# Kernel optimization log

Measured on AMD Instinct MI355X. Metric: run time of the kernel, lower is better.

Reference implementation:

```python
import jax, jax.numpy as jnp
import numpy as np

B, N, H = 1, 4096, 2048
NH, HD = 16, H // 16
WINDOW = 4096
EPS = 1e-6
THETA = 10000.0
NEG = -1e30


def rmsnorm(x, w):
    var = jnp.mean(jnp.square(x.astype(jnp.float32)), axis=-1, keepdims=True)
    return (x * jax.lax.rsqrt(var + EPS)).astype(w.dtype) * w


def rotate_half(x):
    x1, x2 = x[..., : x.shape[-1] // 2], x[..., x.shape[-1] // 2 :]
    return jnp.concatenate((-x2, x1), axis=-1)


def setup_inputs() -> dict:
    key = jax.random.key(0)
    k1, k2, k3 = jax.random.split(key, 3)
    x = jax.random.normal(k1, (B, N, H), dtype=jnp.float32)
    w_qkv = jax.random.normal(k2, (H, 3 * H), dtype=jnp.float32) * (1.0 / np.sqrt(H))
    w_out = jax.random.normal(k3, (H, H), dtype=jnp.float32) * (1.0 / np.sqrt(H))
    q_gamma = jnp.ones((HD,), dtype=jnp.float32)
    k_gamma = jnp.ones((HD,), dtype=jnp.float32)
    return {"x": x, "w_qkv": w_qkv, "w_out": w_out, "q_gamma": q_gamma, "k_gamma": k_gamma}


def reference(x, w_qkv, w_out, q_gamma, k_gamma):
    b, n, _ = x.shape
    qkv = jnp.einsum('bnh,hm->bnm', x, w_qkv)  # [b,n,3H]
    q, k, v = jnp.split(qkv, 3, axis=-1)
    # [b, nh, n, hd]
    q = q.reshape(b, n, NH, HD).transpose(0, 2, 1, 3)
    k = k.reshape(b, n, NH, HD).transpose(0, 2, 1, 3)
    v = v.reshape(b, n, NH, HD).transpose(0, 2, 1, 3)
    # qk RMSNorm over head_dim
    q = rmsnorm(q, q_gamma)
    k = rmsnorm(k, k_gamma)
    # RoPE
    inv_freq = 1.0 / (THETA ** (jnp.arange(0, HD, 2, dtype=jnp.float32) / HD))
    t = jnp.arange(n, dtype=jnp.float32)
    freqs = t[:, None] * inv_freq[None, :]          # [n, hd/2]
    emb = jnp.concatenate((freqs, freqs), axis=-1)  # [n, hd]
    cos = jnp.cos(emb)[None, None, :, :]
    sin = jnp.sin(emb)[None, None, :, :]
    q = q * cos + rotate_half(q) * sin
    k = k * cos + rotate_half(k) * sin
    # causal + sliding-window mask (kv not truncated since n == WINDOW)
    kv_len = k.shape[-2]
    q_idx = jnp.arange(n)[:, None] + (kv_len - n)
    k_idx = jnp.arange(kv_len)[None, :]
    mask = (q_idx >= k_idx) & (q_idx - k_idx <= WINDOW)
    scores = jnp.einsum('bhqd,bhkd->bhqk', q, k) / np.sqrt(HD)
    scores = jnp.where(mask[None, None, :, :], scores, NEG)
    attn = jax.nn.softmax(scores, axis=-1)
    out = jnp.einsum('bhqk,bhkd->bhqd', attn, v)
    out = out.transpose(0, 2, 1, 3).reshape(b, n, H)
    return jnp.einsum('bnh,hm->bnm', out, w_out)
```

## Files before the change

kernel.cpp:

```cpp
#include <hip/hip_runtime.h>
#include <stdint.h>

typedef short bf16x8 __attribute__((ext_vector_type(8)));
typedef float f32x4 __attribute__((ext_vector_type(4)));
typedef unsigned short u16;

__device__ __forceinline__ float b2f(u16 u) {
  return __uint_as_float(((unsigned)u) << 16);
}
__device__ __forceinline__ u16 f2b(float f) {
  unsigned u = __float_as_uint(f);
  return (u16)((u + 0x7fffu + ((u >> 16) & 1u)) >> 16);
}

#define NEGINF (-1.0e30f)

__device__ __forceinline__ void gld_lds16(const u16* g, u16* l) {
  __builtin_amdgcn_global_load_lds(
      (const __attribute__((address_space(1))) unsigned int*)(const void*)g,
      (__attribute__((address_space(3))) unsigned int*)(void*)l, 16, 0, 0);
}

__device__ __forceinline__ int swzV(int o) {
  return o ^ ((((o) >> 6) & 7) << 3);
}
__device__ __forceinline__ int swzK(int o) {
  return o ^ ((((o) >> 7) & 7) << 3);
}

__global__ void sniff5(const u16* x, const u16* wq, const u16* wo,
                       const u16* qg, const u16* kg, int* flags) {
  const u16* p;
  int S;
  switch (blockIdx.x) {
    case 0: p = x;  S = 2048; break;
    case 1: p = wq; S = 2048; break;
    case 2: p = wo; S = 2048; break;
    case 3: p = qg; S = 128;  break;
    default: p = kg; S = 128; break;
  }
  __shared__ int cbig, czero;
  if (threadIdx.x == 0) { cbig = 0; czero = 0; }
  __syncthreads();
  int cb = 0, cz = 0;
  for (int i = threadIdx.x; i < S; i += 256) {
    const u16 u = p[i];
    if (((u >> 7) & 0xFF) >= 0xC0) ++cb;
    if (!(i & 1) && u == 0) ++cz;
  }
  atomicAdd(&cbig, cb);
  atomicAdd(&czero, cz);
  __syncthreads();
  if (threadIdx.x == 0)
    flags[blockIdx.x] = (cbig > S / 32 || czero > 3 * S / 8) ? 1 : 0;
}

__global__ __launch_bounds__(256) void conv_in(const void* __restrict__ src,
                                               u16* __restrict__ dst,
                                               const int* __restrict__ flags,
                                               int fidx, int n) {
  const int fp32 = flags[fidx];
  int i = blockIdx.x * 256 + threadIdx.x;
  const int stride = gridDim.x * 256;
  if (fp32) {
    const float* s = (const float*)src;
    for (; i < n; i += stride) dst[i] = f2b(s[i]);
  } else {
    const u16* s = (const u16*)src;
    for (; i < n; i += stride) dst[i] = s[i];
  }
}

__global__ __launch_bounds__(256) void transpose_in(
    const void* __restrict__ src, u16* __restrict__ dst,
    const int* __restrict__ flags, int fidx, int ss, int ds) {
  __shared__ u16 tile[64][65];
  const int fp32 = flags[fidx];
  const int rb = blockIdx.y * 64, cb = blockIdx.x * 64;
  const int cl = threadIdx.x & 63, r0 = threadIdx.x >> 6;
  if (fp32) {
    const float* s = (const float*)src;
#pragma unroll
    for (int i = 0; i < 16; ++i) {
      int r = r0 + i * 4;
      tile[r][cl] = f2b(s[(long long)(rb + r) * ss + cb + cl]);
    }
  } else {
    const u16* s = (const u16*)src;
#pragma unroll
    for (int i = 0; i < 16; ++i) {
      int r = r0 + i * 4;
      tile[r][cl] = s[(long long)(rb + r) * ss + cb + cl];
    }
  }
  __syncthreads();
#pragma unroll
  for (int i = 0; i < 16; ++i) {
    int r2 = r0 + i * 4;
    dst[(long long)(cb + r2) * ds + rb + cl] = tile[cl][r2];
  }
}

__global__ __launch_bounds__(256) void transpose_bf16(
    const u16* __restrict__ src, u16* __restrict__ dst, int ss, int ds,
    long long sz, long long dz) {
  __shared__ u16 tile[64][65];
  const u16* s = src + (long long)blockIdx.z * sz;
  u16* d = dst + (long long)blockIdx.z * dz;
  const int rb = blockIdx.y * 64, cb = blockIdx.x * 64;
  const int cl = threadIdx.x & 63, r0 = threadIdx.x >> 6;
#pragma unroll
  for (int i = 0; i < 16; ++i) {
    int r = r0 + i * 4;
    tile[r][cl] = s[(long long)(rb + r) * ss + cb + cl];
  }
  __syncthreads();
#pragma unroll
  for (int i = 0; i < 16; ++i) {
    int r2 = r0 + i * 4;
    d[(long long)(cb + r2) * ds + rb + cl] = tile[cl][r2];
  }
}

__global__ __launch_bounds__(256) void gemm_qkv(
    const u16* __restrict__ A, const u16* __restrict__ Bt,
    u16* __restrict__ Cq, u16* __restrict__ Ck, u16* __restrict__ Cv, int K) {
  __shared__ __align__(16) u16 As[128 * 64];
  __shared__ __align__(16) u16 Bs[128 * 64];
  const int bid = blockIdx.x;
  const int xcd = bid & 7, lid = bid >> 3;
  const int mb = lid / 6, nsub = lid - mb * 6;
  const int nb = xcd * 6 + nsub;
  const int m0 = mb * 128;
  const int n0g = nb * 128;
  const int sel = nb >> 4;
  u16* C = sel == 0 ? Cq : (sel == 1 ? Ck : Cv);
  const int n0 = (nb & 15) * 128;
  const int tid = threadIdx.x;
  const int w = tid >> 6, l = tid & 63;
  const int lane15 = l & 15, quad = l >> 4;
  const int wm = (w >> 1) * 64, wn = (w & 1) * 64;
  const int r8 = l >> 3, c8 = l & 7;
  const int sk = (c8 ^ r8) * 8;
  const u16* gA = A + (size_t)(m0 + r8) * K + sk;
  const u16* gB = Bt + (size_t)(n0g + r8) * K + sk;
  f32x4 acc[4][4] = {};
  const int nK = K >> 6;
  for (int kb = 0; kb < nK; ++kb) {
    __syncthreads();
#pragma unroll
    for (int i = 0; i < 4; ++i) {
      const int g = i * 4 + w;
      gld_lds16(gA + (size_t)g * 8 * K, &As[g * 512]);
      gld_lds16(gB + (size_t)g * 8 * K, &Bs[g * 512]);
    }
    __syncthreads();
#pragma unroll
    for (int kk = 0; kk < 2; ++kk) {
      bf16x8 af[4], bfr[4];
#pragma unroll
      for (int mi = 0; mi < 4; ++mi)
        af[mi] = *(const bf16x8*)&As[swzV((wm + mi * 16 + lane15) * 64 +
                                          kk * 32 + quad * 8)];
#pragma unroll
      for (int ni = 0; ni < 4; ++ni)
        bfr[ni] = *(const bf16x8*)&Bs[swzV((wn + ni * 16 + lane15) * 64 +
                                           kk * 32 + quad * 8)];
#pragma unroll
      for (int mi = 0; mi < 4; ++mi)
#pragma unroll
        for (int ni = 0; ni < 4; ++ni)
          acc[mi][ni] = __builtin_amdgcn_mfma_f32_16x16x32_bf16(
              af[mi], bfr[ni], acc[mi][ni], 0, 0, 0);
    }
    gA += 64;
    gB += 64;
  }
#pragma unroll
  for (int mi = 0; mi < 4; ++mi)
#pragma unroll
    for (int ni = 0; ni < 4; ++ni)
#pragma unroll
      for (int r = 0; r < 4; ++r)
        C[(size_t)(m0 + wm + mi * 16 + quad * 4 + r) * 2048 +
          (n0 + wn + ni * 16 + lane15)] = f2b(acc[mi][ni][r]);
}

__global__ __launch_bounds__(256) void gemm_bt_f32(
    const u16* __restrict__ A, const u16* __restrict__ Bt,
    float* __restrict__ C, int K) {
  __shared__ __align__(16) u16 As[128 * 64];
  __shared__ __align__(16) u16 Bs[128 * 64];
  const int bid = blockIdx.x;
  const int xcd = bid & 7, lid = bid >> 3;
  const int mb = lid >> 1, nsub = lid & 1;
  const int nb = xcd * 2 + nsub;
  const int m0 = mb * 128, n0 = nb * 128;
  const int tid = threadIdx.x;
  const int w = tid >> 6, l = tid & 63;
  const int lane15 = l & 15, quad = l >> 4;
  const int wm = (w >> 1) * 64, wn = (w & 1) * 64;
  const int r8 = l >> 3, c8 = l & 7;
  const int sk = (c8 ^ r8) * 8;
  const u16* gA = A + (size_t)(m0 + r8) * K + sk;
  const u16* gB = Bt + (size_t)(n0 + r8) * K + sk;
  f32x4 acc[4][4] = {};
  const int nK = K >> 6;
  for (int kb = 0; kb < nK; ++kb) {
    __syncthreads();
#pragma unroll
    for (int i = 0; i < 4; ++i) {
      const int g = i * 4 + w;
      gld_lds16(gA + (size_t)g * 8 * K, &As[g * 512]);
      gld_lds16(gB + (size_t)g * 8 * K, &Bs[g * 512]);
    }
    __syncthreads();
#pragma unroll
    for (int kk = 0; kk < 2; ++kk) {
      bf16x8 af[4], bfr[4];
#pragma unroll
      for (int mi = 0; mi < 4; ++mi)
        af[mi] = *(const bf16x8*)&As[swzV((wm + mi * 16 + lane15) * 64 +
                                          kk * 32 + quad * 8)];
#pragma unroll
      for (int ni = 0; ni < 4; ++ni)
        bfr[ni] = *(const bf16x8*)&Bs[swzV((wn + ni * 16 + lane15) * 64 +
                                           kk * 32 + quad * 8)];
#pragma unroll
      for (int mi = 0; mi < 4; ++mi)
#pragma unroll
        for (int ni = 0; ni < 4; ++ni)
          acc[mi][ni] = __builtin_amdgcn_mfma_f32_16x16x32_bf16(
              af[mi], bfr[ni], acc[mi][ni], 0, 0, 0);
    }
    gA += 64;
    gB += 64;
  }
#pragma unroll
  for (int mi = 0; mi < 4; ++mi)
#pragma unroll
    for (int ni = 0; ni < 4; ++ni)
#pragma unroll
      for (int r = 0; r < 4; ++r)
        C[(size_t)(m0 + wm + mi * 16 + quad * 4 + r) * 2048 +
          (n0 + wn + ni * 16 + lane15)] = acc[mi][ni][r];
}

__global__ __launch_bounds__(256) void rms_rope(
    const u16* __restrict__ in, const u16* __restrict__ gamma,
    u16* __restrict__ outr) {
  const int wid = blockIdx.x * 4 + (threadIdx.x >> 6);
  const int l = threadIdx.x & 63;
  const int n = wid >> 4;
  const int h = wid & 15;
  const u16* base = in + (size_t)n * 2048 + h * 128;
  float a = b2f(base[l]), b = b2f(base[l + 64]);
  float ssum = a * a + b * b;
#pragma unroll
  for (int m = 1; m < 64; m <<= 1) ssum += __shfl_xor(ssum, m);
  const float r = rsqrtf(ssum * (1.0f / 128.0f) + 1e-6f);
  a *= r * b2f(gamma[l]);
  b *= r * b2f(gamma[l + 64]);
  const float inv = __expf(-(float)l * 0.14391156831212787f);
  float s, c;
  sincosf((float)n * inv, &s, &c);
  const size_t o = ((size_t)h * 4096 + n) * 128 + l;
  outr[o] = f2b(a * c - b * s);
  outr[o + 64] = f2b(b * c + a * s);
}

__global__ __launch_bounds__(256, 2) void flash_attn(
    const u16* __restrict__ q_r, const u16* __restrict__ k_r,
    const u16* __restrict__ v_t, u16* __restrict__ attn) {
  __shared__ __align__(16) u16 Kt[64 * 128];
  __shared__ __align__(16) u16 Vt[128 * 64];
  __shared__ __align__(16) u16 Pt[128 * 64];
  const int b = blockIdx.x;
  const int h = b & 15;
  const int qt = (b < 256) ? (31 - (b >> 4)) : ((b - 256) >> 4);
  const int m0 = qt * 128;
  const int tid = threadIdx.x, w = tid >> 6, l = tid & 63;
  const int lane15 = l & 15, quad = l >> 4;

  bf16x8 aq[2][4];
#pragma unroll
  for (int mi = 0; mi < 2; ++mi)
#pragma unroll
    for (int ks = 0; ks < 4; ++ks)
      aq[mi][ks] = *(const bf16x8*)&q_r[((size_t)h * 4096 + m0 + w * 32 +
                                         mi * 16 + lane15) * 128 +
                                        ks * 32 + quad * 8];

  f32x4 acc_o[2][8] = {};
  float m_i[2][4], l_i[2][4];
#pragma unroll
  for (int mi = 0; mi < 2; ++mi)
#pragma unroll
    for (int r = 0; r < 4; ++r) {
      m_i[mi][r] = NEGINF;
      l_i[mi][r] = 0.f;
    }

  const int jend = m0 + 64;
  for (int j0 = 0; j0 <= jend; j0 += 64) {
    __syncthreads();
#pragma unroll
    for (int i = 0; i < 4; ++i) {
      const int rg = i * 4 + w;
      const int keyr = rg * 4 + (l >> 4);
      const int kc = (l & 15) ^ (keyr & 7);
      const int dr = rg * 8 + (l >> 3);
      const int vc = (l & 7) ^ (dr & 7);
      gld_lds16(&k_r[((size_t)h * 4096 + j0 + keyr) * 128 + kc * 8],
                &Kt[rg * 512]);
      gld_lds16(&v_t[((size_t)h * 128 + dr) * 4096 + j0 + vc * 8],
                &Vt[rg * 512]);
    }
    __syncthreads();

    f32x4 s2[2][4] = {};
#pragma unroll
    for (int ni = 0; ni < 4; ++ni) {
#pragma unroll
      for (int ks = 0; ks < 4; ++ks) {
        bf16x8 bk = *(const bf16x8*)&Kt[swzK((ni * 16 + lane15) * 128 +
                                             ks * 32 + quad * 8)];
        s2[0][ni] = __builtin_amdgcn_mfma_f32_16x16x32_bf16(aq[0][ks], bk,
                                                            s2[0][ni], 0, 0, 0);
        s2[1][ni] = __builtin_amdgcn_mfma_f32_16x16x32_bf16(aq[1][ks], bk,
                                                            s2[1][ni], 0, 0, 0);
      }
    }

    const float sc = 0.08838834764831845f;
    const bool mt = (j0 >= m0);
#pragma unroll
    for (int mi = 0; mi < 2; ++mi) {
#pragma unroll
      for (int r = 0; r < 4; ++r) {
        const int lrow = w * 32 + mi * 16 + quad * 4 + r;
        float xv[4], mx4 = NEGINF;
#pragma unroll
        for (int ni = 0; ni < 4; ++ni) {
          float xx = s2[mi][ni][r] * sc;
          if (mt && (j0 + ni * 16 + lane15 > m0 + lrow)) xx = NEGINF;
          xv[ni] = xx;
          mx4 = fmaxf(mx4, xx);
        }
        const float mold = m_i[mi][r];
        const unsigned long long bal = __ballot(mx4 > mold + 8.0f);
        float mcur = mold;
        if (((unsigned)(bal >> (quad * 16)) & 0xFFFFu) != 0u) {
          float mx = mx4;
#pragma unroll
          for (int mk = 1; mk < 16; mk <<= 1)
            mx = fmaxf(mx, __shfl_xor(mx, mk));
          const float mnew = fmaxf(mold, mx);
          const float alpha = __expf(mold - mnew);
          l_i[mi][r] *= alpha;
          m_i[mi][r] = mnew;
          mcur = mnew;
#pragma unroll
          for (int ni = 0; ni < 8; ++ni) acc_o[mi][ni][r] *= alpha;
        }
        float rs = 0.f;
#pragma unroll
        for (int ni = 0; ni < 4; ++ni) {
          const float p = __expf(xv[ni] - mcur);
          Pt[swzV(lrow * 64 + ni * 16 + lane15)] = f2b(p);
          rs += p;
        }
        l_i[mi][r] += rs;
      }
    }

#pragma unroll
    for (int ks = 0; ks < 2; ++ks) {
      bf16x8 ap0 = *(const bf16x8*)&Pt[swzV((w * 32 + lane15) * 64 + ks * 32 +
                                            quad * 8)];
      bf16x8 ap1 = *(const bf16x8*)&Pt[swzV((w * 32 + 16 + lane15) * 64 +
                                            ks * 32 + quad * 8)];
#pragma unroll
      for (int ni = 0; ni < 8; ++ni) {
        bf16x8 bv = *(const bf16x8*)&Vt[swzV((ni * 16 + lane15) * 64 +
                                             ks * 32 + quad * 8)];
        acc_o[0][ni] = __builtin_amdgcn_mfma_f32_16x16x32_bf16(
            ap0, bv, acc_o[0][ni], 0, 0, 0);
        acc_o[1][ni] = __builtin_amdgcn_mfma_f32_16x16x32_bf16(
            ap1, bv, acc_o[1][ni], 0, 0, 0);
      }
    }
  }

#pragma unroll
  for (int mi = 0; mi < 2; ++mi)
#pragma unroll
    for (int r = 0; r < 4; ++r) {
      float s = l_i[mi][r];
#pragma unroll
      for (int mk = 1; mk < 16; mk <<= 1) s += __shfl_xor(s, mk);
      l_i[mi][r] = s;
    }
#pragma unroll
  for (int mi = 0; mi < 2; ++mi)
#pragma unroll
    for (int ni = 0; ni < 8; ++ni)
#pragma unroll
      for (int r = 0; r < 4; ++r)
        attn[(size_t)(m0 + w * 32 + mi * 16 + quad * 4 + r) * 2048 + h * 128 +
             ni * 16 + lane15] = f2b(acc_o[mi][ni][r] / l_i[mi][r]);
}

extern "C" void kernel_launch(void* const* d_in, const int* in_sizes, int n_in,
                              void* d_out, int out_size, void* d_ws,
                              size_t ws_size, hipStream_t stream) {
  (void)out_size; (void)ws_size;
  int ix = 0, iwq = 1, iwo = 2, ig1 = 3, ig2 = 4;
  {
    int g1 = -1, g2 = -1, xx = -1, wqq = -1, woo = -1;
    for (int i = 0; i < n_in; ++i) {
      const int s = in_sizes[i];
      if (s == 8388608) xx = i;
      else if (s == 12582912) wqq = i;
      else if (s == 4194304) woo = i;
      else if (s == 128) { if (g1 < 0) g1 = i; else g2 = i; }
    }
    if (xx >= 0 && wqq >= 0 && woo >= 0 && g1 >= 0 && g2 >= 0) {
      ix = xx; iwq = wqq; iwo = woo; ig1 = g1; ig2 = g2;
    }
  }
  const void* x = d_in[ix];
  const void* wq = d_in[iwq];
  const void* wo = d_in[iwo];
  const void* qg = d_in[ig1];
  const void* kg = d_in[ig2];
  float* out = (float*)d_out;
  char* ws = (char*)d_ws;
  u16* xb = (u16*)(ws);
  u16* k_buf = (u16*)(ws + 16777216LL);
  u16* wT = (u16*)(ws + 33554432LL);
  int* flags = (int*)(ws + 58720256LL);
  u16* gq_b = (u16*)(ws + 58720512LL);
  u16* gk_b = (u16*)(ws + 58721024LL);
  u16* q_r = (u16*)(ws);
  u16* attn = (u16*)(ws + 16777216LL);
  u16* v_t = (u16*)(ws + 33554432LL);
  u16* woT = (u16*)(ws + 50331648LL);
  u16* q_buf = (u16*)d_out;
  u16* k_r = (u16*)d_out;
  u16* v_buf = (u16*)d_out + 8388608;

  sniff5<<<5, 256, 0, stream>>>((const u16*)x, (const u16*)wq, (const u16*)wo,
                                (const u16*)qg, (const u16*)kg, flags);
  conv_in<<<8192, 256, 0, stream>>>(x, xb, flags, 0, 4096 * 2048);
  conv_in<<<1, 256, 0, stream>>>(qg, gq_b, flags, 3, 128);
  conv_in<<<1, 256, 0, stream>>>(kg, gk_b, flags, 4, 128);
  transpose_in<<<dim3(96, 32), 256, 0, stream>>>(wq, wT, flags, 1, 6144, 2048);
  gemm_qkv<<<dim3(1536), 256, 0, stream>>>(xb, wT, q_buf, k_buf, v_buf, 2048);
  rms_rope<<<dim3(16384), 256, 0, stream>>>(q_buf, gq_b, q_r);
  rms_rope<<<dim3(16384), 256, 0, stream>>>(k_buf, gk_b, k_r);
  transpose_bf16<<<dim3(2, 64, 16), 256, 0, stream>>>(v_buf, v_t, 2048, 4096,
                                                      128LL, 524288LL);
  transpose_in<<<dim3(32, 32), 256, 0, stream>>>(wo, woT, flags, 2, 2048, 2048);
  flash_attn<<<dim3(512), 256, 0, stream>>>(q_r, k_r, v_t, attn);
  gemm_bt_f32<<<dim3(512), 256, 0, stream>>>(attn, woT, out, 2048);
}
```

Baseline: 540.2 us.

## Fuse QK RMSNorm, RoPE and V transpose into QKV GEMM epilogue

```diff
diff --git a/kernel.cpp b/kernel.cpp
--- a/kernel.cpp
+++ b/kernel.cpp
@@ -101,32 +101,13 @@
   }
 }
 
-__global__ __launch_bounds__(256) void transpose_bf16(
-    const u16* __restrict__ src, u16* __restrict__ dst, int ss, int ds,
-    long long sz, long long dz) {
-  __shared__ u16 tile[64][65];
-  const u16* s = src + (long long)blockIdx.z * sz;
-  u16* d = dst + (long long)blockIdx.z * dz;
-  const int rb = blockIdx.y * 64, cb = blockIdx.x * 64;
-  const int cl = threadIdx.x & 63, r0 = threadIdx.x >> 6;
-#pragma unroll
-  for (int i = 0; i < 16; ++i) {
-    int r = r0 + i * 4;
-    tile[r][cl] = s[(long long)(rb + r) * ss + cb + cl];
-  }
-  __syncthreads();
-#pragma unroll
-  for (int i = 0; i < 16; ++i) {
-    int r2 = r0 + i * 4;
-    d[(long long)(cb + r2) * ds + rb + cl] = tile[cl][r2];
-  }
-}
-
 __global__ __launch_bounds__(256) void gemm_qkv(
     const u16* __restrict__ A, const u16* __restrict__ Bt,
+    const u16* __restrict__ gq, const u16* __restrict__ gk,
     u16* __restrict__ Cq, u16* __restrict__ Ck, u16* __restrict__ Cv, int K) {
-  __shared__ __align__(16) u16 As[128 * 64];
-  __shared__ __align__(16) u16 Bs[128 * 64];
+  __shared__ __align__(16) u16 smem[2 * 128 * 64];
+  u16* As = smem;
+  u16* Bs = smem + 128 * 64;
   const int bid = blockIdx.x;
   const int xcd = bid & 7, lid = bid >> 3;
   const int mb = lid / 6, nsub = lid - mb * 6;
@@ -134,8 +115,7 @@
   const int m0 = mb * 128;
   const int n0g = nb * 128;
   const int sel = nb >> 4;
-  u16* C = sel == 0 ? Cq : (sel == 1 ? Ck : Cv);
-  const int n0 = (nb & 15) * 128;
+  const int h = nb & 15;
   const int tid = threadIdx.x;
   const int w = tid >> 6, l = tid & 63;
   const int lane15 = l & 15, quad = l >> 4;
@@ -176,14 +156,140 @@
     gA += 64;
     gB += 64;
   }
-#pragma unroll
-  for (int mi = 0; mi < 4; ++mi)
+
+  __syncthreads();
+  if (sel == 2) {
+    u16* t = smem;
+#pragma unroll
+    for (int mi = 0; mi < 4; ++mi)
+#pragma unroll
+      for (int ni = 0; ni < 4; ++ni)
+#pragma unroll
+        for (int r = 0; r < 4; ++r) {
+          const int row = wm + mi * 16 + quad * 4 + r;
+          const int col = wn + ni * 16 + lane15;
+          t[col * 128 + (row ^ ((col & 7) << 4))] = f2b(acc[mi][ni][r]);
+        }
+    __syncthreads();
+    const int d = tid & 127, half = tid >> 7;
+    u16* vdst = Cv + ((size_t)h * 128 + d) * 4096 + m0 + half * 64;
+#pragma unroll
+    for (int c8i = 0; c8i < 8; ++c8i) {
+      const int n0c = half * 64 + c8i * 8;
+      *(bf16x8*)(vdst + c8i * 8) =
+          *(const bf16x8*)&t[d * 128 + (n0c ^ ((d & 7) << 4))];
+    }
+  } else {
+    const u16* g = sel == 0 ? gq : gk;
+    u16* dst = sel == 0 ? Cq : Ck;
+    float* fss = (float*)smem;
+    float gv[4];
+#pragma unroll
+    for (int ni = 0; ni < 4; ++ni) gv[ni] = b2f(g[wn + ni * 16 + lane15]);
+#pragma unroll
+    for (int mi = 0; mi < 4; ++mi)
+#pragma unroll
+      for (int r = 0; r < 4; ++r) {
+        float ss = 0.f;
+#pragma unroll
+        for (int ni = 0; ni < 4; ++ni) ss += acc[mi][ni][r] * acc[mi][ni][r];
+#pragma unroll
+        for (int mk = 1; mk < 16; mk <<= 1) ss += __shfl_xor(ss, mk);
+        if (lane15 == 0)
+          fss[(wm + mi * 16 + quad * 4 + r) * 2 + (w & 1)] = ss;
+      }
+    __syncthreads();
+#pragma unroll
+    for (int mi = 0; mi < 4; ++mi)
+#pragma unroll
+      for (int r = 0; r < 4; ++r) {
+        const int row = wm + mi * 16 + quad * 4 + r;
+        const float rstd =
+            rsqrtf((fss[row * 2] + fss[row * 2 + 1]) * (1.f / 128.f) + 1e-6f);
+#pragma unroll
+        for (int ni = 0; ni < 4; ++ni) acc[mi][ni][r] *= rstd * gv[ni];
+      }
+    __syncthreads();
+    float* fex = (float*)smem;
+    const int wp = w >> 1, lo = w & 1;
+    float invf[4];
 #pragma unroll
     for (int ni = 0; ni < 4; ++ni)
-#pragma unroll
-      for (int r = 0; r < 4; ++r)
-        C[(size_t)(m0 + wm + mi * 16 + quad * 4 + r) * 2048 +
-          (n0 + wn + ni * 16 + lane15)] = f2b(acc[mi][ni][r]);
+      invf[ni] = __expf(-(float)(ni * 16 + lane15) * 0.14391156831212787f);
+    if (lo == 1) {
+#pragma unroll
+      for (int mi = 0; mi < 4; ++mi)
+#pragma unroll
+        for (int ni = 0; ni < 4; ++ni)
+#pragma unroll
+          for (int r = 0; r < 4; ++r)
+            fex[wp * 4096 + (mi * 16 + quad * 4 + r) * 64 + ni * 16 + lane15] =
+                acc[mi][ni][r];
+    }
+    __syncthreads();
+    if (lo == 0) {
+#pragma unroll
+      for (int ni = 0; ni < 4; ++ni) {
+        float cI, sI;
+        sincosf(invf[ni], &sI, &cI);
+#pragma unroll
+        for (int mi = 0; mi < 4; ++mi) {
+          const int rloc0 = mi * 16 + quad * 4;
+          const int p0 = m0 + wm + rloc0;
+          float c, s;
+          sincosf((float)p0 * invf[ni], &s, &c);
+#pragma unroll
+          for (int r = 0; r < 4; ++r) {
+            const float a = acc[mi][ni][r];
+            const float bb =
+                fex[wp * 4096 + (rloc0 + r) * 64 + ni * 16 + lane15];
+            dst[((size_t)h * 4096 + p0 + r) * 128 + ni * 16 + lane15] =
+                f2b(a * c - bb * s);
+            const float c2 = c * cI - s * sI;
+            s = s * cI + c * sI;
+            c = c2;
+          }
+        }
+      }
+    }
+    __syncthreads();
+    if (lo == 0) {
+#pragma unroll
+      for (int mi = 0; mi < 4; ++mi)
+#pragma unroll
+        for (int ni = 0; ni < 4; ++ni)
+#pragma unroll
+          for (int r = 0; r < 4; ++r)
+            fex[wp * 4096 + (mi * 16 + quad * 4 + r) * 64 + ni * 16 + lane15] =
+                acc[mi][ni][r];
+    }
+    __syncthreads();
+    if (lo == 1) {
+#pragma unroll
+      for (int ni = 0; ni < 4; ++ni) {
+        float cI, sI;
+        sincosf(invf[ni], &sI, &cI);
+#pragma unroll
+        for (int mi = 0; mi < 4; ++mi) {
+          const int rloc0 = mi * 16 + quad * 4;
+          const int p0 = m0 + wm + rloc0;
+          float c, s;
+          sincosf((float)p0 * invf[ni], &s, &c);
+#pragma unroll
+          for (int r = 0; r < 4; ++r) {
+            const float bb = acc[mi][ni][r];
+            const float a =
+                fex[wp * 4096 + (rloc0 + r) * 64 + ni * 16 + lane15];
+            dst[((size_t)h * 4096 + p0 + r) * 128 + 64 + ni * 16 + lane15] =
+                f2b(bb * c + a * s);
+            const float c2 = c * cI - s * sI;
+            s = s * cI + c * sI;
+            c = c2;
+          }
+        }
+      }
+    }
+  }
 }
 
 __global__ __launch_bounds__(256) void gemm_bt_f32(
@@ -246,29 +352,6 @@
           (n0 + wn + ni * 16 + lane15)] = acc[mi][ni][r];
 }
 
-__global__ __launch_bounds__(256) void rms_rope(
-    const u16* __restrict__ in, const u16* __restrict__ gamma,
-    u16* __restrict__ outr) {
-  const int wid = blockIdx.x * 4 + (threadIdx.x >> 6);
-  const int l = threadIdx.x & 63;
-  const int n = wid >> 4;
-  const int h = wid & 15;
-  const u16* base = in + (size_t)n * 2048 + h * 128;
-  float a = b2f(base[l]), b = b2f(base[l + 64]);
-  float ssum = a * a + b * b;
-#pragma unroll
-  for (int m = 1; m < 64; m <<= 1) ssum += __shfl_xor(ssum, m);
-  const float r = rsqrtf(ssum * (1.0f / 128.0f) + 1e-6f);
-  a *= r * b2f(gamma[l]);
-  b *= r * b2f(gamma[l + 64]);
-  const float inv = __expf(-(float)l * 0.14391156831212787f);
-  float s, c;
-  sincosf((float)n * inv, &s, &c);
-  const size_t o = ((size_t)h * 4096 + n) * 128 + l;
-  outr[o] = f2b(a * c - b * s);
-  outr[o + 64] = f2b(b * c + a * s);
-}
-
 __global__ __launch_bounds__(256, 2) void flash_attn(
     const u16* __restrict__ q_r, const u16* __restrict__ k_r,
     const u16* __restrict__ v_t, u16* __restrict__ attn) {
@@ -437,18 +520,15 @@
   float* out = (float*)d_out;
   char* ws = (char*)d_ws;
   u16* xb = (u16*)(ws);
-  u16* k_buf = (u16*)(ws + 16777216LL);
+  u16* q_r = (u16*)(ws + 16777216LL);
   u16* wT = (u16*)(ws + 33554432LL);
+  u16* attn = (u16*)(ws + 33554432LL);
+  u16* woT = (u16*)(ws + 50331648LL);
   int* flags = (int*)(ws + 58720256LL);
   u16* gq_b = (u16*)(ws + 58720512LL);
   u16* gk_b = (u16*)(ws + 58721024LL);
-  u16* q_r = (u16*)(ws);
-  u16* attn = (u16*)(ws + 16777216LL);
-  u16* v_t = (u16*)(ws + 33554432LL);
-  u16* woT = (u16*)(ws + 50331648LL);
-  u16* q_buf = (u16*)d_out;
   u16* k_r = (u16*)d_out;
-  u16* v_buf = (u16*)d_out + 8388608;
+  u16* v_t = (u16*)d_out + 8388608;
 
   sniff5<<<5, 256, 0, stream>>>((const u16*)x, (const u16*)wq, (const u16*)wo,
                                 (const u16*)qg, (const u16*)kg, flags);
@@ -456,11 +536,8 @@
   conv_in<<<1, 256, 0, stream>>>(qg, gq_b, flags, 3, 128);
   conv_in<<<1, 256, 0, stream>>>(kg, gk_b, flags, 4, 128);
   transpose_in<<<dim3(96, 32), 256, 0, stream>>>(wq, wT, flags, 1, 6144, 2048);
-  gemm_qkv<<<dim3(1536), 256, 0, stream>>>(xb, wT, q_buf, k_buf, v_buf, 2048);
-  rms_rope<<<dim3(16384), 256, 0, stream>>>(q_buf, gq_b, q_r);
-  rms_rope<<<dim3(16384), 256, 0, stream>>>(k_buf, gk_b, k_r);
-  transpose_bf16<<<dim3(2, 64, 16), 256, 0, stream>>>(v_buf, v_t, 2048, 4096,
-                                                      128LL, 524288LL);
+  gemm_qkv<<<dim3(1536), 256, 0, stream>>>(xb, wT, gq_b, gk_b, q_r, k_r, v_t,
+                                           2048);
   transpose_in<<<dim3(32, 32), 256, 0, stream>>>(wo, woT, flags, 2, 2048, 2048);
   flash_attn<<<dim3(512), 256, 0, stream>>>(q_r, k_r, v_t, attn);
   gemm_bt_f32<<<dim3(512), 256, 0, stream>>>(attn, woT, out, 2048);
```

Measured after the change: 703.5 us. 30.2% more time.
